# Optimization experiments

Hardware: AMD Instinct MI355X
Metric: run time of the kernel (lower is better)

The kernel has to match this reference:

```python
import jax, jax.numpy as jnp
import numpy as np

B, S, D = 2, 2048, 2048
H, DN, DR, DV = 16, 128, 64, 128   # heads, qk_nope, qk_rope, v_head
Q_LORA, KV_LORA = 1536, 512
DQ = DN + DR                        # qk_head_dim = 192
EPS = 1e-6


def setup_inputs() -> dict:
    key = jax.random.key(0)
    ks = jax.random.split(key, 8)
    s = 0.02  # weight init scale
    hidden_states = jax.random.normal(ks[0], (B, S, D), jnp.float32)
    # RoPE tables (non-interleaved HF style: cat(freqs, freqs)) per position
    inv_freq = 1.0 / (10000.0 ** (np.arange(0, DR, 2, dtype=np.float32) / DR))
    freqs = np.arange(S, dtype=np.float32)[:, None] * inv_freq[None, :]  # [S, DR/2]
    emb = np.concatenate([freqs, freqs], axis=-1)                        # [S, DR]
    cos = jnp.broadcast_to(jnp.asarray(np.cos(emb)), (B, S, DR))
    sin = jnp.broadcast_to(jnp.asarray(np.sin(emb)), (B, S, DR))
    return {
        'hidden_states': hidden_states,
        'cos': cos, 'sin': sin,
        'Wqa': jax.random.normal(ks[1], (D, Q_LORA), jnp.float32) * s,
        'qa_ln_w': jnp.ones((Q_LORA,), jnp.float32),
        'Wqb': jax.random.normal(ks[2], (Q_LORA, H * DQ), jnp.float32) * s,
        'Wkva': jax.random.normal(ks[3], (D, KV_LORA + DR), jnp.float32) * s,
        'kva_ln_w': jnp.ones((KV_LORA,), jnp.float32),
        'Wkvb': jax.random.normal(ks[4], (KV_LORA, H * (DN + DV)), jnp.float32) * s,
        'Wo': jax.random.normal(ks[5], (H * DV, D), jnp.float32) * s,
    }


def _rmsnorm(x, w):
    xf = x.astype(jnp.float32)
    var = jnp.mean(xf * xf, axis=-1, keepdims=True)
    return w * (xf * jax.lax.rsqrt(var + EPS)).astype(x.dtype)


def _rotate_half(x):
    h = x.shape[-1] // 2
    return jnp.concatenate([-x[..., h:], x[..., :h]], axis=-1)


def reference(hidden_states, cos, sin, Wqa, qa_ln_w, Wqb, Wkva, kva_ln_w, Wkvb, Wo):
    b, s, _ = hidden_states.shape
    scaling = DQ ** -0.5

    # Q path: down-proj -> RMSNorm -> up-proj -> [b, H, s, DQ]
    q = _rmsnorm(hidden_states @ Wqa, qa_ln_w) @ Wqb
    q = q.reshape(b, s, H, DQ).transpose(0, 2, 1, 3)
    q_pass, q_rot = q[..., :DN], q[..., DN:]

    # KV path: joint down-proj -> split latent / shared rope key
    ckv = hidden_states @ Wkva                       # [b, s, KV_LORA + DR]
    k_lat, k_rot = ckv[..., :KV_LORA], ckv[..., KV_LORA:]
    kv = _rmsnorm(k_lat, kva_ln_w) @ Wkvb            # [b, s, H*(DN+DV)]
    kv = kv.reshape(b, s, H, DN + DV).transpose(0, 2, 1, 3)
    k_pass, v = kv[..., :DN], kv[..., DN:]

    # decoupled RoPE on q_rot and the single shared k_rot head
    k_rot = k_rot[:, None, :, :]                     # [b, 1, s, DR]
    c, si = cos[:, None], sin[:, None]               # unsqueeze_dim=1
    q_rot = q_rot * c + _rotate_half(q_rot) * si
    k_rot = k_rot * c + _rotate_half(k_rot) * si
    k_rot = jnp.broadcast_to(k_rot, (b, H, s, DR))

    Q = jnp.concatenate([q_pass, q_rot], axis=-1)    # [b, H, s, DQ]
    K = jnp.concatenate([k_pass, k_rot], axis=-1)

    scores = jnp.einsum('bhqd,bhkd->bhqk', Q, K) * scaling
    neg = jnp.finfo(jnp.float32).min
    causal = jnp.where(jnp.tril(jnp.ones((s, s), bool)), 0.0, neg)
    scores = scores + causal
    w = jax.nn.softmax(scores.astype(jnp.float32), axis=-1).astype(Q.dtype)

    out = jnp.einsum('bhqk,bhkd->bhqd', w, v)
    out = out.transpose(0, 2, 1, 3).reshape(b, s, H * DV)
    return out @ Wo
```

## Files before the change

### kernel.cpp

```cpp
#include <hip/hip_runtime.h>
#include <math.h>

#define BB 2
#define SS 2048
#define DD 2048
#define HH 16
#define DN 128
#define DR 64
#define DV 128
#define QL 1536
#define KVL 512
#define DQ 192
#define CKVS 640
#define KVD 256
#define NCAT 2176
#define EPSF 1e-6f

typedef short bfrag __attribute__((ext_vector_type(8)));
typedef float facc  __attribute__((ext_vector_type(4)));

__device__ __forceinline__ ushort f2bf(float f) {
    union { float f; unsigned u; } v; v.f = f;
    unsigned r = v.u + 0x7fffu + ((v.u >> 16) & 1u);
    return (ushort)(r >> 16);
}
__device__ __forceinline__ float bf2f(ushort u) {
    union { unsigned u; float f; } v; v.u = ((unsigned)u) << 16;
    return v.f;
}
__device__ __forceinline__ float wave_red_sum(float v) {
    #pragma unroll
    for (int o = 32; o > 0; o >>= 1) v += __shfl_down(v, o);
    return v;
}
__device__ __forceinline__ void gl2lds16(const ushort* g, ushort* l) {
    __builtin_amdgcn_global_load_lds(
        (const __attribute__((address_space(1))) void*)g,
        (__attribute__((address_space(3))) void*)l, 16, 0, 0);
}
__device__ __forceinline__ void storeC(float* c, float v)  { *c = v; }
__device__ __forceinline__ void storeC(ushort* c, float v) { *c = f2bf(v); }

__global__ __launch_bounds__(256) void castf2bf(const float* __restrict__ x,
                                                ushort* __restrict__ y) {
    const int i = blockIdx.x * 256 + threadIdx.x;
    const float4 v = ((const float4*)x)[i];
    ushort4 o;
    o.x = f2bf(v.x); o.y = f2bf(v.y); o.z = f2bf(v.z); o.w = f2bf(v.w);
    ((ushort4*)y)[i] = o;
}

struct WtBatch {
    const float* src[5];
    ushort* dst[5];
    int K[5];
    int N[5];
    int nx[5];
    int base[6];
};
__global__ __launch_bounds__(256) void wtrans_b(WtBatch d) {
    __shared__ float tile[32][33];
    int bid = blockIdx.x;
    int seg = 0;
    while (bid >= d.base[seg + 1]) ++seg;
    const int l = bid - d.base[seg];
    const int nx = d.nx[seg];
    const int bx = l % nx, by = l / nx;
    const float* W = d.src[seg];
    ushort* Wt = d.dst[seg];
    const int K = d.K[seg], N = d.N[seg];
    const int k0 = by * 32, n0 = bx * 32;
    const int t = threadIdx.x;
    const int tx = t & 31, ty = t >> 5;
    #pragma unroll
    for (int r = 0; r < 4; ++r) {
        const int n = n0 + tx;
        tile[ty + r * 8][tx] =
            (n < N) ? W[(size_t)(k0 + ty + r * 8) * N + n] : 0.f;
    }
    __syncthreads();
    #pragma unroll
    for (int r = 0; r < 4; ++r) {
        const int n = n0 + ty + r * 8;
        Wt[(size_t)n * K + k0 + tx] = f2bf(tile[tx][ty + r * 8]);
    }
}

#define GEMM_CORE(A_, Bt_, K_)                                               \
    __shared__ ushort Asu[128 * 32];                                         \
    __shared__ ushort Bsu[128 * 32];                                         \
    const int t    = threadIdx.x;                                            \
    const int lane = t & 63;                                                 \
    const int wave = t >> 6;                                                 \
    const int quad = lane >> 4;                                              \
    const int lrow = lane & 15;                                              \
    const int m0 = blockIdx.y * 128;                                         \
    const int n0 = blockIdx.x * 128;                                         \
    const int mw = (wave >> 1) * 64;                                         \
    const int nw = (wave & 1) * 64;                                          \
    int srow[2], scol[2], soff[2];                                           \
    _Pragma("unroll")                                                        \
    for (int p = 0; p < 2; ++p) {                                            \
        const int c = (wave * 2 + p) * 64 + lane;                            \
        srow[p] = c >> 2;                                                    \
        scol[p] = (c & 3) * 8;                                               \
        soff[p] = (wave * 2 + p) * 512;                                      \
    }                                                                        \
    facc acc[4][4];                                                          \
    _Pragma("unroll")                                                        \
    for (int i = 0; i < 4; ++i)                                              \
        _Pragma("unroll")                                                    \
        for (int j = 0; j < 4; ++j) acc[i][j] = (facc)(0.f);                 \
    for (int k0 = 0; k0 < (K_); k0 += 32) {                                  \
        _Pragma("unroll")                                                    \
        for (int p = 0; p < 2; ++p) {                                        \
            gl2lds16((A_)  + (size_t)(m0 + srow[p]) * (K_) + k0 + scol[p],   \
                     Asu + soff[p]);                                         \
            gl2lds16((Bt_) + (size_t)(n0 + srow[p]) * (K_) + k0 + scol[p],   \
                     Bsu + soff[p]);                                         \
        }                                                                    \
        __syncthreads();                                                     \
        bfrag a[4], b[4];                                                    \
        _Pragma("unroll")                                                    \
        for (int i = 0; i < 4; ++i)                                          \
            a[i] = *(const bfrag*)&Asu[(mw + i * 16 + lrow) * 32 + quad * 8];\
        _Pragma("unroll")                                                    \
        for (int j = 0; j < 4; ++j)                                          \
            b[j] = *(const bfrag*)&Bsu[(nw + j * 16 + lrow) * 32 + quad * 8];\
        _Pragma("unroll")                                                    \
        for (int i = 0; i < 4; ++i)                                          \
            _Pragma("unroll")                                                \
            for (int j = 0; j < 4; ++j)                                      \
                acc[i][j] = __builtin_amdgcn_mfma_f32_16x16x32_bf16(         \
                    a[i], b[j], acc[i][j], 0, 0, 0);                         \
        __syncthreads();                                                     \
    }

template <typename OUT>
__global__ __launch_bounds__(256) void gemm_bf(const ushort* __restrict__ A,
                                               const ushort* __restrict__ Bt,
                                               OUT* __restrict__ C,
                                               int M, int N, int K) {
    GEMM_CORE(A, Bt, K)
    #pragma unroll
    for (int i = 0; i < 4; ++i) {
        #pragma unroll
        for (int j = 0; j < 4; ++j) {
            const int row = m0 + mw + i * 16 + quad * 4;
            const int col = n0 + nw + j * 16 + lrow;
            #pragma unroll
            for (int r = 0; r < 4; ++r)
                storeC(&C[(size_t)(row + r) * N + col], acc[i][j][r]);
        }
    }
}

__global__ __launch_bounds__(256) void gemmA(const ushort* __restrict__ A,
                                             const ushort* __restrict__ Bt,
                                             ushort* __restrict__ qa,
                                             ushort* __restrict__ ckv) {
    GEMM_CORE(A, Bt, DD)
    const bool isq = (n0 < QL);
    #pragma unroll
    for (int i = 0; i < 4; ++i) {
        #pragma unroll
        for (int j = 0; j < 4; ++j) {
            const int row = m0 + mw + i * 16 + quad * 4;
            const int col = n0 + nw + j * 16 + lrow;
            #pragma unroll
            for (int r = 0; r < 4; ++r) {
                if (isq) qa[(size_t)(row + r) * QL + col] = f2bf(acc[i][j][r]);
                else     ckv[(size_t)(row + r) * CKVS + col - QL] = f2bf(acc[i][j][r]);
            }
        }
    }
}

__global__ __launch_bounds__(256) void gemmQ(const ushort* __restrict__ A,
                                             const ushort* __restrict__ Bt,
                                             ushort* __restrict__ Qbuf) {
    GEMM_CORE(A, Bt, QL)
    const float scaling = 0.07216878364870323f;
    #pragma unroll
    for (int i = 0; i < 4; ++i) {
        #pragma unroll
        for (int j = 0; j < 4; ++j) {
            const int row = m0 + mw + i * 16 + quad * 4;
            const int col = n0 + nw + j * 16 + lrow;
            const int h = col / DQ, d = col - h * DQ;
            #pragma unroll
            for (int r = 0; r < 4; ++r) {
                const int tok = row + r;
                const int b = tok >> 11, s = tok & (SS - 1);
                Qbuf[((size_t)(b * HH + h) * SS + s) * DQ + d] =
                    f2bf(acc[i][j][r] * scaling);
            }
        }
    }
}

__global__ __launch_bounds__(256) void rmsnorm_bf_ip(ushort* __restrict__ x,
                                                     const float* __restrict__ w,
                                                     int n) {
    ushort* xr = x + (size_t)blockIdx.x * n;
    const int t = threadIdx.x;
    float ss = 0.f;
    for (int i = t; i < n; i += 256) { float v = bf2f(xr[i]); ss += v * v; }
    ss = wave_red_sum(ss);
    __shared__ float red[4];
    const int lane = t & 63, wid = t >> 6;
    if (lane == 0) red[wid] = ss;
    __syncthreads();
    const float tot = red[0] + red[1] + red[2] + red[3];
    const float scale = rsqrtf(tot / (float)n + EPSF);
    for (int i = t; i < n; i += 256) xr[i] = f2bf(w[i] * bf2f(xr[i]) * scale);
}

__global__ __launch_bounds__(256) void rmsnorm_kv(const ushort* __restrict__ x,
                                                  const float* __restrict__ w,
                                                  ushort* __restrict__ y,
                                                  ushort* __restrict__ krb,
                                                  const float* __restrict__ cosb,
                                                  const float* __restrict__ sinb) {
    const int row = blockIdx.x;
    const ushort* xr = x + (size_t)row * CKVS;
    ushort* yr = y + (size_t)row * KVL;
    const int t = threadIdx.x;
    if (t < 64) {
        const int p = t;
        const ushort* kin = xr + KVL;
        const float c  = cosb[(size_t)row * DR + p];
        const float sn = sinb[(size_t)row * DR + p];
        const float self = bf2f(kin[p]);
        const float partner = bf2f(kin[p < 32 ? p + 32 : p - 32]);
        const float v = (p < 32) ? (self * c - partner * sn)
                                 : (self * c + partner * sn);
        krb[(size_t)row * DR + p] = f2bf(v);
    }
    float ss = 0.f;
    for (int i = t; i < KVL; i += 256) { float v = bf2f(xr[i]); ss += v * v; }
    ss = wave_red_sum(ss);
    __shared__ float red[4];
    const int lane = t & 63, wid = t >> 6;
    if (lane == 0) red[wid] = ss;
    __syncthreads();
    const float tot = red[0] + red[1] + red[2] + red[3];
    const float scale = rsqrtf(tot / (float)KVL + EPSF);
    for (int i = t; i < KVL; i += 256) yr[i] = f2bf(w[i] * bf2f(xr[i]) * scale);
}

__global__ __launch_bounds__(256) void qrope(ushort* __restrict__ Qbuf,
                                             const float* __restrict__ cosb,
                                             const float* __restrict__ sinb) {
    const int tok = blockIdx.x;
    const int b = tok >> 11, s = tok & (SS - 1);
    const int t = threadIdx.x;
    const int p = t & 31, hh = t >> 5;
    const float c0 = cosb[(size_t)tok * DR + p];
    const float s0 = sinb[(size_t)tok * DR + p];
    const float c1 = cosb[(size_t)tok * DR + p + 32];
    const float s1 = sinb[(size_t)tok * DR + p + 32];
    #pragma unroll
    for (int it = 0; it < 2; ++it) {
        const int h = hh + it * 8;
        ushort* base = Qbuf + ((size_t)(b * HH + h) * SS + s) * DQ + DN;
        const float x0 = bf2f(base[p]), x1 = bf2f(base[p + 32]);
        base[p]      = f2bf(x0 * c0 - x1 * s0);
        base[p + 32] = f2bf(x1 * c1 + x0 * s1);
    }
}

__global__ __launch_bounds__(256) void vprep(const ushort* __restrict__ kv_bf,
                                             ushort* __restrict__ Vtb) {
    __shared__ ushort tile[32][33];
    const int kp0 = blockIdx.x * 32, dv0 = blockIdx.y * 32, bh = blockIdx.z;
    const int b = bh / HH, h = bh - b * HH;
    const int t = threadIdx.x, tx = t & 31, ty = t >> 5;
    #pragma unroll
    for (int r = 0; r < 4; ++r)
        tile[ty + r * 8][tx] =
            kv_bf[(size_t)(b * SS + kp0 + ty + r * 8) * (HH * KVD) + h * KVD + DN + dv0 + tx];
    __syncthreads();
    #pragma unroll
    for (int r = 0; r < 4; ++r)
        Vtb[((size_t)bh * DV + dv0 + ty + r * 8) * SS + kp0 + tx] = tile[tx][ty + r * 8];
}

__global__ __launch_bounds__(256, 2) void fattn_mfma(
    const ushort* __restrict__ Qb,
    const ushort* __restrict__ kvb,
    const ushort* __restrict__ krb,
    const ushort* __restrict__ Vt,
    ushort* __restrict__ o)
{
    const int h  = blockIdx.y;
    const int b  = blockIdx.z;
    const int qt = b ? (15 - (int)blockIdx.x) : (int)blockIdx.x;
    const int bh = b * HH + h;
    const int q0 = qt * 128;
    const int t    = threadIdx.x;
    const int lane = t & 63;
    const int wave = t >> 6;
    const int quad = lane >> 4;
    const int n    = lane & 15;
    const int wstrip = wave * 16;

    __shared__ ushort Ksu[6 * 64 * 32];
    __shared__ ushort Vtu[2 * 128 * 32];
    __shared__ ushort Psu[2 * 128 * 40];

    const ushort* vbase = Vt + (size_t)bh * DV * SS;

    bfrag aQ[2][6];
    #pragma unroll
    for (int sp = 0; sp < 2; ++sp) {
        const ushort* qrow = Qb + ((size_t)bh * SS + q0 + sp * 64 + wstrip + n) * DQ;
        #pragma unroll
        for (int kb = 0; kb < 6; ++kb)
            aQ[sp][kb] = *(const bfrag*)(qrow + kb * 32 + quad * 8);
    }

    facc oacc[2][8];
    float lp[2][4];
    #pragma unroll
    for (int sp = 0; sp < 2; ++sp) {
        #pragma unroll
        for (int jd = 0; jd < 8; ++jd) oacc[sp][jd] = (facc)(0.f);
        #pragma unroll
        for (int r = 0; r < 4; ++r) lp[sp][r] = 0.f;
    }

    const int nkt = 2 * qt + 2;
    for (int kt = 0; kt < nkt; ++kt) {
        const int k0 = kt * 64;

        #pragma unroll
        for (int i = 0; i < 6; ++i) {
            const int g = wave + 4 * i;
            const int kb = g >> 2;
            const int rem = (g & 3) * 64 + lane;
            const int row = rem >> 2, sub = rem & 3;
            const int tok = b * SS + k0 + row;
            const ushort* src = (kb < 4)
                ? kvb + (size_t)tok * (HH * KVD) + h * KVD + kb * 32 + sub * 8
                : krb + (size_t)tok * DR + (kb - 4) * 32 + sub * 8;
            gl2lds16(src, Ksu + g * 512);
        }
        #pragma unroll
        for (int i = 0; i < 4; ++i) {
            const int g = wave + 4 * i;
            const int kb2 = g >> 3;
            const int rem = (g & 7) * 64 + lane;
            const int dv = rem >> 2, sub = rem & 3;
            gl2lds16(vbase + (size_t)dv * SS + k0 + kb2 * 32 + sub * 8,
                     Vtu + g * 512);
        }
        __syncthreads();

        facc s[2][4];
        #pragma unroll
        for (int sp = 0; sp < 2; ++sp)
            #pragma unroll
            for (int j = 0; j < 4; ++j) s[sp][j] = (facc)(0.f);
        #pragma unroll
        for (int kb = 0; kb < 6; ++kb) {
            #pragma unroll
            for (int j = 0; j < 4; ++j) {
                const bfrag bk =
                    *(const bfrag*)&Ksu[kb * 2048 + (j * 16 + n) * 32 + quad * 8];
                s[0][j] = __builtin_amdgcn_mfma_f32_16x16x32_bf16(aQ[0][kb], bk, s[0][j], 0, 0, 0);
                s[1][j] = __builtin_amdgcn_mfma_f32_16x16x32_bf16(aQ[1][kb], bk, s[1][j], 0, 0, 0);
            }
        }

        #pragma unroll
        for (int sp = 0; sp < 2; ++sp) {
            const int rowg0 = q0 + sp * 64 + wstrip + quad * 4;
            #pragma unroll
            for (int j = 0; j < 4; ++j) {
                const int kpos = k0 + j * 16 + n;
                #pragma unroll
                for (int r = 0; r < 4; ++r) {
                    float p = (kpos <= rowg0 + r) ? __expf(s[sp][j][r]) : 0.f;
                    lp[sp][r] += p;
                    Psu[(j >> 1) * 5120 + (sp * 64 + wstrip + quad * 4 + r) * 40
                        + (j & 1) * 16 + n] = f2bf(p);
                }
            }
        }

        #pragma unroll
        for (int kb2 = 0; kb2 < 2; ++kb2) {
            const bfrag aP0 = *(const bfrag*)&Psu[kb2 * 5120 + (wstrip + n) * 40 + quad * 8];
            const bfrag aP1 = *(const bfrag*)&Psu[kb2 * 5120 + (64 + wstrip + n) * 40 + quad * 8];
            #pragma unroll
            for (int jd = 0; jd < 8; ++jd) {
                const bfrag bV = *(const bfrag*)&Vtu[kb2 * 4096 + (jd * 16 + n) * 32 + quad * 8];
                oacc[0][jd] = __builtin_amdgcn_mfma_f32_16x16x32_bf16(aP0, bV, oacc[0][jd], 0, 0, 0);
                oacc[1][jd] = __builtin_amdgcn_mfma_f32_16x16x32_bf16(aP1, bV, oacc[1][jd], 0, 0, 0);
            }
        }
        __syncthreads();
    }

    #pragma unroll
    for (int sp = 0; sp < 2; ++sp) {
        #pragma unroll
        for (int r = 0; r < 4; ++r) {
            float v = lp[sp][r];
            #pragma unroll
            for (int msk = 1; msk < 16; msk <<= 1) v += __shfl_xor(v, msk);
            const float inv = 1.f / v;
            ushort* op = o + (size_t)(b * SS + q0 + sp * 64 + wstrip + quad * 4 + r)
                             * (HH * DV) + h * DV;
            #pragma unroll
            for (int jd = 0; jd < 8; ++jd)
                op[jd * 16 + n] = f2bf(oacc[sp][jd][r] * inv);
        }
    }
}

extern "C" void kernel_launch(void* const* d_in, const int* in_sizes, int n_in,
                              void* d_out, int out_size, void* d_ws, size_t ws_size,
                              hipStream_t stream) {
    const float* hs    = (const float*)d_in[0];
    const float* cosb  = (const float*)d_in[1];
    const float* sinb  = (const float*)d_in[2];
    const float* Wqa   = (const float*)d_in[3];
    const float* qa_w  = (const float*)d_in[4];
    const float* Wqb   = (const float*)d_in[5];
    const float* Wkva  = (const float*)d_in[6];
    const float* kva_w = (const float*)d_in[7];
    const float* Wkvb  = (const float*)d_in[8];
    const float* Wo    = (const float*)d_in[9];
    float* out = (float*)d_out;

    const int T = BB * SS;

    char* w = (char*)d_ws;
    auto alloc = [&](size_t bytes) {
        void* r = (void*)w;
        w += (bytes + 255) & ~(size_t)255;
        return r;
    };
    ushort* hs_bf  = (ushort*)alloc((size_t)T * DD * 2);
    ushort* Wcat   = (ushort*)alloc((size_t)NCAT * DD * 2);
    ushort* Wqbt   = (ushort*)alloc((size_t)(HH * DQ) * QL * 2);
    ushort* Wkvbt  = (ushort*)alloc((size_t)(HH * KVD) * KVL * 2);
    ushort* Wot    = (ushort*)alloc((size_t)DD * DD * 2);
    ushort* qa_bf  = (ushort*)alloc((size_t)T * QL * 2);
    ushort* Qbuf   = (ushort*)alloc((size_t)T * HH * DQ * 2);
    ushort* ckv_bf = (ushort*)alloc((size_t)T * CKVS * 2);
    ushort* kvn_bf = (ushort*)alloc((size_t)T * KVL * 2);
    ushort* kv_bf  = (ushort*)alloc((size_t)T * HH * KVD * 2);
    ushort* krb    = (ushort*)alloc((size_t)T * DR * 2);
    ushort* Vtb    = Wcat;
    ushort* ao_bf  = hs_bf;

    castf2bf<<<(T * DD / 4) / 256, 256, 0, stream>>>(hs, hs_bf);
    WtBatch wb;
    wb.src[0] = Wqa;  wb.dst[0] = Wcat;                      wb.K[0] = DD;  wb.N[0] = QL;       wb.nx[0] = 48;
    wb.src[1] = Wkva; wb.dst[1] = Wcat + (size_t)QL * DD;    wb.K[1] = DD;  wb.N[1] = KVL + DR; wb.nx[1] = 20;
    wb.src[2] = Wqb;  wb.dst[2] = Wqbt;                      wb.K[2] = QL;  wb.N[2] = HH * DQ;  wb.nx[2] = 96;
    wb.src[3] = Wkvb; wb.dst[3] = Wkvbt;                     wb.K[3] = KVL; wb.N[3] = HH * KVD; wb.nx[3] = 128;
    wb.src[4] = Wo;   wb.dst[4] = Wot;                       wb.K[4] = DD;  wb.N[4] = DD;       wb.nx[4] = 64;
    wb.base[0] = 0;
    wb.base[1] = wb.base[0] + wb.nx[0] * (DD / 32);
    wb.base[2] = wb.base[1] + wb.nx[1] * (DD / 32);
    wb.base[3] = wb.base[2] + wb.nx[2] * (QL / 32);
    wb.base[4] = wb.base[3] + wb.nx[3] * (KVL / 32);
    wb.base[5] = wb.base[4] + wb.nx[4] * (DD / 32);
    wtrans_b<<<wb.base[5], 256, 0, stream>>>(wb);

    gemmA<<<dim3(NCAT / 128, T / 128), 256, 0, stream>>>(hs_bf, Wcat, qa_bf, ckv_bf);
    rmsnorm_bf_ip<<<T, 256, 0, stream>>>(qa_bf, qa_w, QL);
    gemmQ<<<dim3((HH * DQ) / 128, T / 128), 256, 0, stream>>>(qa_bf, Wqbt, Qbuf);
    qrope<<<T, 256, 0, stream>>>(Qbuf, cosb, sinb);
    rmsnorm_kv<<<T, 256, 0, stream>>>(ckv_bf, kva_w, kvn_bf, krb, cosb, sinb);
    gemm_bf<ushort><<<dim3((HH * KVD) / 128, T / 128), 256, 0, stream>>>(kvn_bf, Wkvbt, kv_bf, T, HH * KVD, KVL);
    vprep<<<dim3(SS / 32, DV / 32, BB * HH), 256, 0, stream>>>(kv_bf, Vtb);
    fattn_mfma<<<dim3(16, HH, BB), 256, 0, stream>>>(Qbuf, kv_bf, krb, Vtb, ao_bf);
    gemm_bf<float><<<dim3(DD / 128, T / 128), 256, 0, stream>>>(ao_bf, Wot, out, T, DD, DD);
}
```

Before: 484.1 us.

## Replace 128x128 GEMMs with 256x256 double-buffered swizzled LDS pipelined GEMM

Replaces every bf16 GEMM with a 256x256-tile, 512-thread kernel that uses a 64-deep K step. Global-to-LDS loads are double-buffered and interleaved with MFMA phases. The kernel adds an XOR-swizzled LDS layout to avoid bank conflicts, s_setprio scheduling hints and an XCD-aware block remap. The goal is more data reuse per tile and less load latency exposed to the matrix cores. The concatenated weight buffer is padded to 2304 columns to fit the larger tile, with guarded stores. Risks are fewer blocks per GPU for the smaller GEMMs (e.g. 128 blocks for the output projection) and heavy LDS use (128KB) that limits occupancy.

```diff
diff --git a/kernel.cpp b/kernel.cpp
--- a/kernel.cpp
+++ b/kernel.cpp
@@ -14,6 +14,7 @@
 #define CKVS 640
 #define KVD 256
 #define NCAT 2176
+#define NCATP 2304
 #define EPSF 1e-6f
 
 typedef short bfrag __attribute__((ext_vector_type(8)));
@@ -86,114 +87,179 @@
     }
 }
 
-#define GEMM_CORE(A_, Bt_, K_)                                               \
-    __shared__ ushort Asu[128 * 32];                                         \
-    __shared__ ushort Bsu[128 * 32];                                         \
-    const int t    = threadIdx.x;                                            \
-    const int lane = t & 63;                                                 \
-    const int wave = t >> 6;                                                 \
-    const int quad = lane >> 4;                                              \
-    const int lrow = lane & 15;                                              \
-    const int m0 = blockIdx.y * 128;                                         \
-    const int n0 = blockIdx.x * 128;                                         \
-    const int mw = (wave >> 1) * 64;                                         \
-    const int nw = (wave & 1) * 64;                                          \
-    int srow[2], scol[2], soff[2];                                           \
-    _Pragma("unroll")                                                        \
-    for (int p = 0; p < 2; ++p) {                                            \
-        const int c = (wave * 2 + p) * 64 + lane;                            \
-        srow[p] = c >> 2;                                                    \
-        scol[p] = (c & 3) * 8;                                               \
-        soff[p] = (wave * 2 + p) * 512;                                      \
-    }                                                                        \
-    facc acc[4][4];                                                          \
+
+__device__ __forceinline__ void stage_half(const ushort* __restrict__ G,
+                                           int ldg, int grow0, int kcol0,
+                                           ushort* Lr, int wave, int lane) {
+    const int r0   = lane >> 3;
+    const int slot = (lane & 7) ^ r0;
+    const ushort* s0 = G + (size_t)(grow0 + wave * 16 + r0) * ldg + kcol0 + slot * 8;
+    gl2lds16(s0,                    Lr + wave * 1024);
+    gl2lds16(s0 + (size_t)8 * ldg,  Lr + wave * 1024 + 512);
+}
+
+#define PH_PRE  do { __builtin_amdgcn_sched_barrier(0);                      \
+                     __builtin_amdgcn_s_barrier();                           \
+                     asm volatile("s_waitcnt lgkmcnt(0)" ::: "memory");      \
+                     __builtin_amdgcn_sched_barrier(0);                      \
+                     __builtin_amdgcn_s_setprio(1); } while (0)
+#define PH_POST do { __builtin_amdgcn_s_setprio(0);                          \
+                     __builtin_amdgcn_sched_barrier(0);                      \
+                     __builtin_amdgcn_s_barrier(); } while (0)
+
+#define MFMA16(RB)                                                           \
     _Pragma("unroll")                                                        \
     for (int i = 0; i < 4; ++i)                                              \
         _Pragma("unroll")                                                    \
-        for (int j = 0; j < 4; ++j) acc[i][j] = (facc)(0.f);                 \
-    for (int k0 = 0; k0 < (K_); k0 += 32) {                                  \
-        _Pragma("unroll")                                                    \
-        for (int p = 0; p < 2; ++p) {                                        \
-            gl2lds16((A_)  + (size_t)(m0 + srow[p]) * (K_) + k0 + scol[p],   \
-                     Asu + soff[p]);                                         \
-            gl2lds16((Bt_) + (size_t)(n0 + srow[p]) * (K_) + k0 + scol[p],   \
-                     Bsu + soff[p]);                                         \
-        }                                                                    \
-        __syncthreads();                                                     \
-        bfrag a[4], b[4];                                                    \
-        _Pragma("unroll")                                                    \
-        for (int i = 0; i < 4; ++i)                                          \
-            a[i] = *(const bfrag*)&Asu[(mw + i * 16 + lrow) * 32 + quad * 8];\
-        _Pragma("unroll")                                                    \
         for (int j = 0; j < 4; ++j)                                          \
-            b[j] = *(const bfrag*)&Bsu[(nw + j * 16 + lrow) * 32 + quad * 8];\
-        _Pragma("unroll")                                                    \
-        for (int i = 0; i < 4; ++i)                                          \
-            _Pragma("unroll")                                                \
-            for (int j = 0; j < 4; ++j)                                      \
-                acc[i][j] = __builtin_amdgcn_mfma_f32_16x16x32_bf16(         \
-                    a[i], b[j], acc[i][j], 0, 0, 0);                         \
-        __syncthreads();                                                     \
-    }
-
-template <typename OUT>
-__global__ __launch_bounds__(256) void gemm_bf(const ushort* __restrict__ A,
-                                               const ushort* __restrict__ Bt,
-                                               OUT* __restrict__ C,
-                                               int M, int N, int K) {
-    GEMM_CORE(A, Bt, K)
-    #pragma unroll
-    for (int i = 0; i < 4; ++i) {
-        #pragma unroll
-        for (int j = 0; j < 4; ++j) {
-            const int row = m0 + mw + i * 16 + quad * 4;
-            const int col = n0 + nw + j * 16 + lrow;
+            acc[(RB) + i][j] = __builtin_amdgcn_mfma_f32_16x16x32_bf16(      \
+                a[i], b[j], acc[(RB) + i][j], 0, 0, 0);
+
+#define GEMM256_CORE(A_, Bt_, K_, NBX_)                                       \
+    __shared__ ushort L[65536];                           \
+    const int t    = threadIdx.x;                                             \
+    const int lane = t & 63;                                                  \
+    const int wave = t >> 6;                                                  \
+    const int wm   = wave >> 2;                                               \
+    const int wn   = wave & 3;                                                \
+    const int quad = lane >> 4;                                               \
+    const int lrow = lane & 15;                                               \
+    int wg = (int)blockIdx.x;                                                 \
+    { const int cpx = (int)gridDim.x >> 3; wg = (wg & 7) * cpx + (wg >> 3); } \
+    const int bx = wg % (NBX_), by = wg / (NBX_);                             \
+    const int m0 = by * 256, n0 = bx * 256;                                   \
+    const int s0x8  = (quad ^ (lrow & 7)) * 8;       \
+    const int s1x8  = s0x8 ^ 32;                   \
+    const int abase = lrow * 64;                                              \
+    const int bbase = (wn & 1) * 4096 + lrow * 64;                            \
+    facc acc[8][4];                                                           \
+    _Pragma("unroll")                                                         \
+    for (int i = 0; i < 8; ++i)                                               \
+        _Pragma("unroll")                                                     \
+        for (int j = 0; j < 4; ++j) acc[i][j] = (facc)(0.f);                  \
+    const int nk = (K_) >> 6;                                                 \
+                  \
+    stage_half((A_),  (K_), m0,        0, L,         wave, lane);             \
+    stage_half((A_),  (K_), m0 + 128,  0, L + 8192,  wave, lane);             \
+    stage_half((Bt_), (K_), n0,        0, L + 16384, wave, lane);             \
+    stage_half((Bt_), (K_), n0 + 128,  0, L + 24576, wave, lane);             \
+    stage_half((Bt_), (K_), n0,       64, L + 49152, wave, lane);             \
+    stage_half((Bt_), (K_), n0 + 128, 64, L + 57344, wave, lane);             \
+    asm volatile("s_waitcnt vmcnt(4)" ::: "memory");                          \
+    __builtin_amdgcn_s_barrier();                                             \
+    for (int kt = 0; kt < nk; ++kt) {                                         \
+        const int p = kt & 1;                                                 \
+        ushort* LA = L + p * 32768 + wm * 8192;                               \
+        ushort* LB = L + p * 32768 + 16384 + (wn >> 1) * 8192;                \
+        ushort* Lq = L + (p ^ 1) * 32768;                                     \
+        const int kn = (kt + 1) * 64;                                         \
+        bfrag a[4], b[4];                                                     \
+                                           \
+        _Pragma("unroll")                                                     \
+        for (int i = 0; i < 4; ++i)                                           \
+            a[i] = *(const bfrag*)(LA + i * 1024 + abase + s0x8);             \
+        _Pragma("unroll")                                                     \
+        for (int j = 0; j < 4; ++j)                                           \
+            b[j] = *(const bfrag*)(LB + bbase + j * 1024 + s0x8);             \
+        if (kt + 1 < nk) stage_half((A_), (K_), m0, kn, Lq, wave, lane);      \
+        PH_PRE;                                                               \
+        MFMA16(0)                                                             \
+        PH_POST;                                                              \
+                                \
+        _Pragma("unroll")                                                     \
+        for (int i = 0; i < 4; ++i)                                           \
+            a[i] = *(const bfrag*)(LA + (4 + i) * 1024 + abase + s0x8);       \
+        if (kt + 1 < nk)                                                      \
+            stage_half((A_), (K_), m0 + 128, kn, Lq + 8192, wave, lane);      \
+        PH_PRE;                                                               \
+        MFMA16(4)                                                             \
+        PH_POST;                                                              \
+                                           \
+        _Pragma("unroll")                                                     \
+        for (int i = 0; i < 4; ++i)                                           \
+            a[i] = *(const bfrag*)(LA + i * 1024 + abase + s1x8);             \
+        _Pragma("unroll")                                                     \
+        for (int j = 0; j < 4; ++j)                                           \
+            b[j] = *(const bfrag*)(LB + bbase + j * 1024 + s1x8);             \
+        PH_PRE;                                                               \
+        MFMA16(0)                                                             \
+        PH_POST;                                                              \
+             \
+        _Pragma("unroll")                                                     \
+        for (int i = 0; i < 4; ++i)                                           \
+            a[i] = *(const bfrag*)(LA + (4 + i) * 1024 + abase + s1x8);       \
+        if (kt + 2 < nk) {                                                    \
+            stage_half((Bt_), (K_), n0,       kn + 64,                        \
+                       L + p * 32768 + 16384, wave, lane);                    \
+            stage_half((Bt_), (K_), n0 + 128, kn + 64,                        \
+                       L + p * 32768 + 24576, wave, lane);                    \
+            asm volatile("s_waitcnt vmcnt(4)" ::: "memory");                  \
+        } else {                                                              \
+            asm volatile("s_waitcnt vmcnt(0)" ::: "memory");                  \
+        }                                                                     \
+        PH_PRE;                                                               \
+        MFMA16(4)                                                             \
+        PH_POST;                                                              \
+    }
+
+template <typename OUT, int K, int NBX, int NOUT>
+__global__ __launch_bounds__(512, 2) void gemm256(const ushort* __restrict__ A,
+                                                  const ushort* __restrict__ Bt,
+                                                  OUT* __restrict__ C) {
+    GEMM256_CORE(A, Bt, K, NBX)
+    #pragma unroll
+    for (int m = 0; m < 8; ++m) {
+        const int row = m0 + wm * 128 + m * 16 + quad * 4;
+        #pragma unroll
+        for (int nf = 0; nf < 4; ++nf) {
+            const int col = n0 + wn * 64 + nf * 16 + lrow;
             #pragma unroll
             for (int r = 0; r < 4; ++r)
-                storeC(&C[(size_t)(row + r) * N + col], acc[i][j][r]);
-        }
-    }
-}
-
-__global__ __launch_bounds__(256) void gemmA(const ushort* __restrict__ A,
-                                             const ushort* __restrict__ Bt,
-                                             ushort* __restrict__ qa,
-                                             ushort* __restrict__ ckv) {
-    GEMM_CORE(A, Bt, DD)
-    const bool isq = (n0 < QL);
-    #pragma unroll
-    for (int i = 0; i < 4; ++i) {
-        #pragma unroll
-        for (int j = 0; j < 4; ++j) {
-            const int row = m0 + mw + i * 16 + quad * 4;
-            const int col = n0 + nw + j * 16 + lrow;
+                storeC(&C[(size_t)(row + r) * NOUT + col], acc[m][nf][r]);
+        }
+    }
+}
+
+__global__ __launch_bounds__(512, 2) void gemmA256(const ushort* __restrict__ A,
+                                                   const ushort* __restrict__ Bt,
+                                                   ushort* __restrict__ qa,
+                                                   ushort* __restrict__ ckv) {
+    GEMM256_CORE(A, Bt, DD, 9)
+    #pragma unroll
+    for (int m = 0; m < 8; ++m) {
+        const int row = m0 + wm * 128 + m * 16 + quad * 4;
+        #pragma unroll
+        for (int nf = 0; nf < 4; ++nf) {
+            const int col = n0 + wn * 64 + nf * 16 + lrow;
             #pragma unroll
             for (int r = 0; r < 4; ++r) {
-                if (isq) qa[(size_t)(row + r) * QL + col] = f2bf(acc[i][j][r]);
-                else     ckv[(size_t)(row + r) * CKVS + col - QL] = f2bf(acc[i][j][r]);
+                if (col < QL)
+                    qa[(size_t)(row + r) * QL + col] = f2bf(acc[m][nf][r]);
+                else if (col < NCAT)
+                    ckv[(size_t)(row + r) * CKVS + col - QL] = f2bf(acc[m][nf][r]);
             }
         }
     }
 }
 
-__global__ __launch_bounds__(256) void gemmQ(const ushort* __restrict__ A,
-                                             const ushort* __restrict__ Bt,
-                                             ushort* __restrict__ Qbuf) {
-    GEMM_CORE(A, Bt, QL)
+__global__ __launch_bounds__(512, 2) void gemmQ256(const ushort* __restrict__ A,
+                                                   const ushort* __restrict__ Bt,
+                                                   ushort* __restrict__ Qbuf) {
+    GEMM256_CORE(A, Bt, QL, 12)
     const float scaling = 0.07216878364870323f;
     #pragma unroll
-    for (int i = 0; i < 4; ++i) {
-        #pragma unroll
-        for (int j = 0; j < 4; ++j) {
-            const int row = m0 + mw + i * 16 + quad * 4;
-            const int col = n0 + nw + j * 16 + lrow;
+    for (int m = 0; m < 8; ++m) {
+        const int row = m0 + wm * 128 + m * 16 + quad * 4;
+        #pragma unroll
+        for (int nf = 0; nf < 4; ++nf) {
+            const int col = n0 + wn * 64 + nf * 16 + lrow;
             const int h = col / DQ, d = col - h * DQ;
             #pragma unroll
             for (int r = 0; r < 4; ++r) {
                 const int tok = row + r;
                 const int b = tok >> 11, s = tok & (SS - 1);
                 Qbuf[((size_t)(b * HH + h) * SS + s) * DQ + d] =
-                    f2bf(acc[i][j][r] * scaling);
+                    f2bf(acc[m][nf][r] * scaling);
             }
         }
     }
@@ -444,7 +510,7 @@
         return r;
     };
     ushort* hs_bf  = (ushort*)alloc((size_t)T * DD * 2);
-    ushort* Wcat   = (ushort*)alloc((size_t)NCAT * DD * 2);
+    ushort* Wcat   = (ushort*)alloc((size_t)NCATP * DD * 2);
     ushort* Wqbt   = (ushort*)alloc((size_t)(HH * DQ) * QL * 2);
     ushort* Wkvbt  = (ushort*)alloc((size_t)(HH * KVD) * KVL * 2);
     ushort* Wot    = (ushort*)alloc((size_t)DD * DD * 2);
@@ -472,13 +538,13 @@
     wb.base[5] = wb.base[4] + wb.nx[4] * (DD / 32);
     wtrans_b<<<wb.base[5], 256, 0, stream>>>(wb);
 
-    gemmA<<<dim3(NCAT / 128, T / 128), 256, 0, stream>>>(hs_bf, Wcat, qa_bf, ckv_bf);
+    gemmA256<<<dim3(9 * 16), 512, 0, stream>>>(hs_bf, Wcat, qa_bf, ckv_bf);
     rmsnorm_bf_ip<<<T, 256, 0, stream>>>(qa_bf, qa_w, QL);
-    gemmQ<<<dim3((HH * DQ) / 128, T / 128), 256, 0, stream>>>(qa_bf, Wqbt, Qbuf);
+    gemmQ256<<<dim3(12 * 16), 512, 0, stream>>>(qa_bf, Wqbt, Qbuf);
     qrope<<<T, 256, 0, stream>>>(Qbuf, cosb, sinb);
     rmsnorm_kv<<<T, 256, 0, stream>>>(ckv_bf, kva_w, kvn_bf, krb, cosb, sinb);
-    gemm_bf<ushort><<<dim3((HH * KVD) / 128, T / 128), 256, 0, stream>>>(kvn_bf, Wkvbt, kv_bf, T, HH * KVD, KVL);
+    gemm256<ushort, KVL, 16, HH * KVD><<<dim3(16 * 16), 512, 0, stream>>>(kvn_bf, Wkvbt, kv_bf);
     vprep<<<dim3(SS / 32, DV / 32, BB * HH), 256, 0, stream>>>(kv_bf, Vtb);
     fattn_mfma<<<dim3(16, HH, BB), 256, 0, stream>>>(Qbuf, kv_bf, krb, Vtb, ao_bf);
-    gemm_bf<float><<<dim3(DD / 128, T / 128), 256, 0, stream>>>(ao_bf, Wot, out, T, DD, DD);
-}
+    gemm256<float, DD, 8, DD><<<dim3(8 * 16), 512, 0, stream>>>(ao_bf, Wot, out);
+}
```

Measured after the change: 451.3 us. 1.07x faster.
